# Performance work log

Measured on AMD Instinct MI355X. Metric: run time of the kernel, lower is better.

Reference implementation:

```python
import jax, jax.numpy as jnp
import numpy as np

B, S, D, C = 16, 1024, 768, 2


def setup_inputs() -> dict:
    key = jax.random.key(0)
    ks = jax.random.split(key, 6)
    sc = 1.0 / np.sqrt(D)
    return {
        "tokens": jax.random.normal(ks[0], (B, S, D), jnp.float32),
        "Wk": jax.random.normal(ks[1], (D, D), jnp.float32) * sc,
        "bk": jnp.zeros((D,), jnp.float32),
        "Wq": jax.random.normal(ks[2], (D, D), jnp.float32) * sc,
        "bq": jnp.zeros((D,), jnp.float32),
        "Wv": jax.random.normal(ks[3], (D, D), jnp.float32) * sc,
        "bv": jnp.zeros((D,), jnp.float32),
        "ln_g": jnp.ones((S, D), jnp.float32),
        "ln_b": jnp.zeros((S, D), jnp.float32),
        "W_sgsa": jax.random.normal(ks[4], (D, 1), jnp.float32) * sc,
        "b_sgsa": jnp.zeros((1,), jnp.float32),
        "W_fnn": jax.random.normal(ks[5], (4 * D, C), jnp.float32) * (1.0 / np.sqrt(4 * D)),
        "b_fnn": jnp.zeros((C,), jnp.float32),
    }


def reference(tokens, Wk, bk, Wq, bq, Wv, bv, ln_g, ln_b, W_sgsa, b_sgsa, W_fnn, b_fnn):
    fact = 1.0 / jnp.sqrt(jnp.asarray(D, tokens.dtype))
    # --- token-wise single-head attention ---
    K = tokens @ Wk + bk                                  # [B,S,D]
    Q = tokens @ Wq + bq
    V = tokens @ Wv + bv
    att = jax.nn.softmax(jnp.einsum('bsd,btd->bst', Q, K) * fact, axis=-1)  # [B,S,S]
    out = jnp.einsum('bst,btd->bsd', att, V)              # [B,S,D]
    # --- LayerNorm over last two dims (S,D) jointly, eps=1e-8 ---
    mu = jnp.mean(out, axis=(1, 2), keepdims=True)
    var = jnp.var(out, axis=(1, 2), keepdims=True)
    out_ln = (out - mu) / jnp.sqrt(var + 1e-8) * ln_g + ln_b
    # --- feature-wise attention (same K/Q/V weights, transposed bmm) ---
    K_N = out_ln @ Wk + bk
    Q_N = out_ln @ Wq + bq
    V_N = out_ln @ Wv + bv
    att_N = jax.nn.softmax(jnp.einsum('bsd,bse->bde', Q_N, K_N) * fact, axis=-1)  # [B,D,D]
    out_N = jnp.einsum('bsd,bde->bse', V_N, att_N)        # [B,S,D]
    # --- SGSA gating ---
    gate = out_N @ W_sgsa + b_sgsa                        # [B,S,1]
    out_sgsa = gate * out_N                               # [B,S,D]
    # --- concat, dual pooling, FC ---
    cat = jnp.concatenate([tokens, out_sgsa], axis=2)     # [B,S,2D]
    pooled = jnp.concatenate([jnp.mean(cat, axis=1), jnp.max(cat, axis=1)], axis=1)  # [B,4D]
    return pooled @ W_fnn + b_fnn                         # [B,C]
```

## Files before the change

### kernel.cpp

```cpp
#include <hip/hip_runtime.h>

#define BB 16
#define SS 1024
#define DD 768

typedef _Float16 f16x4 __attribute__((ext_vector_type(4)));
typedef _Float16 f16x8 __attribute__((ext_vector_type(8)));
typedef float f32x4 __attribute__((ext_vector_type(4)));

__device__ __forceinline__ void gload_lds16(const void* g, void* l) {
  __builtin_amdgcn_global_load_lds(
      (const __attribute__((address_space(1))) unsigned int*)g,
      (__attribute__((address_space(3))) unsigned int*)l, 16, 0, 0);
}

template<int OUTM, int BIAS>
__global__ __launch_bounds__(512) void gemm256(
    const _Float16* __restrict__ A, long long aB,
    const _Float16* __restrict__ Bt, long long bB,
    const float* __restrict__ bias, int biasB,
    void* __restrict__ Cv, long long cB,
    float* __restrict__ aux,
    int M, int N, int K)
{
  __shared__ __attribute__((aligned(16))) _Float16 lds[65536];
  const int t = threadIdx.x;
  int z, m0, n0;
  if (OUTM == 3 || OUTM == 4) {
    const int lin = blockIdx.x + 9 * blockIdx.y;
    const int xcd = lin & 7, idx = lin >> 3;
    const int mt  = xcd * 8 + idx / 9;
    const int zn  = idx % 9;
    z  = zn / 3;
    n0 = (zn % 3) * 256;
    m0 = mt * 256;
  } else {
    z = blockIdx.z;
    m0 = blockIdx.x * 256;
    n0 = blockIdx.y * 256;
  }
  const _Float16* Ab = A + (size_t)z * aB;
  const _Float16* Bb = Bt + (size_t)z * bB;

  const int l = t & 63, w = t >> 6;
  const int wr = (w >> 2) * 128, wc = (w & 3) * 64;
  const int lrow = l & 15, kq = l >> 4;
  const int p2v = lrow >> 1;
  const int qread = ((lrow & 1) << 2) | (kq ^ (p2v & 3));
  const int fragoff = p2v * 128 + qread * 16;

  const int sp = t >> 3, sq = t & 7;
  const int srow = 2 * sp + (sq >> 2);
  const int schk = (sq & 3) ^ (sp & 3);
  const size_t ldK = (size_t)K * 2;
  const char* pA0 = (const char*)Ab + (size_t)(m0 + srow) * ldK + schk * 16;
  const char* pA1 = pA0 + (size_t)128 * ldK;
  const char* pB0 = (const char*)Bb + (size_t)(n0 + srow) * ldK + schk * 16;
  const char* pB1 = pB0 + (size_t)128 * ldK;
  char* const ldsb = (char*)lds;
  const int dstt = t * 16;

  auto stg = [&](int mat, int s, int T, int sd) {
    const char* g0 = (mat ? pB0 : pA0) + (size_t)T * 128 + s * 64;
    const char* g1 = (mat ? pB1 : pA1) + (size_t)T * 128 + s * 64;
    char* d = ldsb + sd * 65536 + mat * 32768 + s * 16384 + dstt;
    gload_lds16(g0, d);
    gload_lds16(g1, d + 8192);
  };

  f32x4 acc[8][4] = {};
  f16x8 b0[4], b1[4], a00[4], a01[4], a10[4], a11[4];

  stg(0, 0, 0, 0); stg(1, 0, 0, 0); stg(0, 1, 0, 0); stg(1, 1, 0, 0);

  const int NT = K >> 6;
  for (int T = 0; T < NT; ++T) {
    const int sd = T & 1, sn = sd ^ 1;
    const char* Abase = ldsb + sd * 65536;
    const char* Bbase = Abase + 32768;
    const bool pf = (T + 1) < NT;

    asm volatile("s_waitcnt vmcnt(0)" ::: "memory");
    __builtin_amdgcn_s_barrier();
    asm volatile("" ::: "memory");
    if (pf) {
      stg(0, 0, T + 1, sn); stg(1, 0, T + 1, sn);
      stg(0, 1, T + 1, sn); stg(1, 1, T + 1, sn);
    }

    #pragma unroll
    for (int n = 0; n < 4; n++)
      b0[n]  = *(const f16x8*)(Bbase + (wc + n * 16) * 64 + fragoff);
    #pragma unroll
    for (int mi = 0; mi < 4; mi++)
      a00[mi] = *(const f16x8*)(Abase + (wr + mi * 16) * 64 + fragoff);
    #pragma unroll
    for (int mi = 0; mi < 4; mi++)
      a01[mi] = *(const f16x8*)(Abase + (wr + 64 + mi * 16) * 64 + fragoff);
    #pragma unroll
    for (int n = 0; n < 4; n++)
      b1[n]  = *(const f16x8*)(Bbase + 16384 + (wc + n * 16) * 64 + fragoff);
    #pragma unroll
    for (int mi = 0; mi < 4; mi++)
      a10[mi] = *(const f16x8*)(Abase + 16384 + (wr + mi * 16) * 64 + fragoff);
    #pragma unroll
    for (int mi = 0; mi < 4; mi++)
      a11[mi] = *(const f16x8*)(Abase + 16384 + (wr + 64 + mi * 16) * 64 + fragoff);

    __builtin_amdgcn_s_setprio(1);
    #pragma unroll
    for (int mi = 0; mi < 4; mi++)
      #pragma unroll
      for (int n = 0; n < 4; n++)
        acc[mi][n] = __builtin_amdgcn_mfma_f32_16x16x32_f16(a00[mi], b0[n], acc[mi][n], 0, 0, 0);
    #pragma unroll
    for (int mi = 0; mi < 4; mi++)
      #pragma unroll
      for (int n = 0; n < 4; n++)
        acc[4 + mi][n] = __builtin_amdgcn_mfma_f32_16x16x32_f16(a01[mi], b0[n], acc[4 + mi][n], 0, 0, 0);
    #pragma unroll
    for (int mi = 0; mi < 4; mi++)
      #pragma unroll
      for (int n = 0; n < 4; n++)
        acc[mi][n] = __builtin_amdgcn_mfma_f32_16x16x32_f16(a10[mi], b1[n], acc[mi][n], 0, 0, 0);
    #pragma unroll
    for (int mi = 0; mi < 4; mi++)
      #pragma unroll
      for (int n = 0; n < 4; n++)
        acc[4 + mi][n] = __builtin_amdgcn_mfma_f32_16x16x32_f16(a11[mi], b1[n], acc[4 + mi][n], 0, 0, 0);
    __builtin_amdgcn_s_setprio(0);
  }

  const int crow = (l >> 4) * 4, ccol = l & 15;
  #pragma unroll
  for (int m = 0; m < 8; ++m) {
    const int rq = m0 + wr + (m >> 2) * 64 + (m & 3) * 16 + crow;
    #pragma unroll
    for (int n = 0; n < 4; ++n) {
      const int c = n0 + wc + n * 16 + ccol;
      const float bv = BIAS ? bias[(size_t)z * biasB + c] : 0.0f;
      if (OUTM == 0) {
        float* C = (float*)Cv + (size_t)z * cB;
        #pragma unroll
        for (int j = 0; j < 4; j++)
          C[(size_t)(rq + j) * N + c] = acc[m][n][j] + bv;
      } else if (OUTM == 5 || OUTM == 6) {
        _Float16* C = (_Float16*)Cv + (size_t)z * cB;
        #pragma unroll
        for (int j = 0; j < 4; j++)
          C[(size_t)(rq + j) * N + c] = (_Float16)(acc[m][n][j] + bv);
      } else {
        _Float16* C = (_Float16*)Cv + (size_t)z * cB;
        const bool tr = (OUTM == 3) ? (z == 2) : (z < 2);
        if (tr) {
          const int bq = rq >> 10, s = rq & 1023;
          f16x4 o;
          #pragma unroll
          for (int j = 0; j < 4; j++) o[j] = (_Float16)(acc[m][n][j] + bv);
          *(f16x4*)&C[((size_t)(bq * N + c) << 10) + s] = o;
        } else {
          #pragma unroll
          for (int j = 0; j < 4; j++)
            C[(size_t)(rq + j) * N + c] = (_Float16)(acc[m][n][j] + bv);
        }
      }
    }
  }

  if (OUTM == 6) {
    float ls = 0.0f, lq = 0.0f;
    #pragma unroll
    for (int m = 0; m < 8; ++m)
      #pragma unroll
      for (int n = 0; n < 4; ++n)
        #pragma unroll
        for (int j = 0; j < 4; j++) {
          const float v = acc[m][n][j];
          ls += v; lq += v * v;
        }
    __syncthreads();
    float* red = (float*)lds;
    red[t] = ls; red[512 + t] = lq;
    __syncthreads();
    #pragma unroll
    for (int off = 256; off > 0; off >>= 1) {
      if (t < off) { red[t] += red[t + off]; red[512 + t] += red[512 + t + off]; }
      __syncthreads();
    }
    if (t == 0) {
      const int chunk = blockIdx.x * 3 + blockIdx.y;
      aux[(z * 12 + chunk) * 2]     = red[0];
      aux[(z * 12 + chunk) * 2 + 1] = red[512];
    }
  }
}

__global__ __launch_bounds__(256) void cast_pool(const float* __restrict__ tokens,
                                                 _Float16* __restrict__ tok_h,
                                                 float* __restrict__ tpart)
{
  const int b = blockIdx.y, ch = blockIdx.x, t = threadIdx.x;
  float s0 = 0, s1 = 0, s2 = 0;
  float x0 = -3.4e38f, x1 = -3.4e38f, x2 = -3.4e38f;
  const size_t rowbase = ((size_t)b * SS + ch * 32) * DD;
  for (int i = 0; i < 32; i++) {
    const float* tr = tokens + rowbase + (size_t)i * DD;
    _Float16* hw = tok_h + rowbase + (size_t)i * DD;
    float t0 = tr[t], t1 = tr[t + 256], t2 = tr[t + 512];
    hw[t] = (_Float16)t0; hw[t + 256] = (_Float16)t1; hw[t + 512] = (_Float16)t2;
    s0 += t0; s1 += t1; s2 += t2;
    x0 = fmaxf(x0, t0); x1 = fmaxf(x1, t1); x2 = fmaxf(x2, t2);
  }
  float* pb = tpart + (size_t)(b * 32 + ch) * 1536;
  pb[t] = s0;        pb[t + 256] = s1;        pb[t + 512] = s2;
  pb[768 + t] = x0;  pb[768 + t + 256] = x1;  pb[768 + t + 512] = x2;
}

__global__ __launch_bounds__(256) void transpose_f2h(const float* __restrict__ in,
                                                     _Float16* __restrict__ outp, int R, int C)
{
  __shared__ float tile[32][33];
  const int r0 = blockIdx.y * 32, c0 = blockIdx.x * 32;
  const int tx = threadIdx.x & 31, ty = threadIdx.x >> 5;
  #pragma unroll
  for (int i = 0; i < 4; i++)
    tile[ty + i * 8][tx] = in[(size_t)(r0 + ty + i * 8) * C + c0 + tx];
  __syncthreads();
  #pragma unroll
  for (int i = 0; i < 4; i++)
    outp[(size_t)(c0 + ty + i * 8) * R + r0 + tx] = (_Float16)tile[tx][ty + i * 8];
}

__global__ __launch_bounds__(256) void transpose_b2h(const _Float16* __restrict__ in, long long inB,
                                                     _Float16* __restrict__ outp, long long outB,
                                                     int R, int C)
{
  __shared__ _Float16 tile[32][33];
  const _Float16* ib = in + (size_t)blockIdx.z * inB;
  _Float16* ob = outp + (size_t)blockIdx.z * outB;
  const int r0 = blockIdx.y * 32, c0 = blockIdx.x * 32;
  const int tx = threadIdx.x & 31, ty = threadIdx.x >> 5;
  #pragma unroll
  for (int i = 0; i < 4; i++)
    tile[ty + i * 8][tx] = ib[(size_t)(r0 + ty + i * 8) * C + c0 + tx];
  __syncthreads();
  #pragma unroll
  for (int i = 0; i < 4; i++)
    ob[(size_t)(c0 + ty + i * 8) * R + r0 + tx] = tile[tx][ty + i * 8];
}

__global__ void pack_bias(const float* __restrict__ a, const float* __restrict__ b,
                          const float* __restrict__ c, float* __restrict__ o)
{
  int t = blockIdx.x * 256 + threadIdx.x;
  if (t < 768) o[t] = a[t];
  else if (t < 1536) o[t] = b[t - 768];
  else if (t < 2304) o[t] = c[t - 1536];
}

template<int VPT>
__global__ __launch_bounds__(256) void softmax_f2h(const float* __restrict__ X,
                                                   _Float16* __restrict__ Y,
                                                   int L, float scale)
{
  const size_t base = (size_t)blockIdx.x * L;
  const int t = threadIdx.x;
  float v[VPT];
  float m = -3.4e38f;
  #pragma unroll
  for (int j = 0; j < VPT; j++) { v[j] = X[base + t + j * 256]; m = fmaxf(m, v[j]); }
  __shared__ float red[256];
  red[t] = m; __syncthreads();
  #pragma unroll
  for (int off = 128; off > 0; off >>= 1) {
    if (t < off) red[t] = fmaxf(red[t], red[t + off]);
    __syncthreads();
  }
  m = red[0]; __syncthreads();
  float s = 0.0f;
  #pragma unroll
  for (int j = 0; j < VPT; j++) { v[j] = __expf((v[j] - m) * scale); s += v[j]; }
  red[t] = s; __syncthreads();
  #pragma unroll
  for (int off = 128; off > 0; off >>= 1) {
    if (t < off) red[t] += red[t + off];
    __syncthreads();
  }
  const float inv = 1.0f / red[0];
  #pragma unroll
  for (int j = 0; j < VPT; j++) Y[base + t + j * 256] = (_Float16)(v[j] * inv);
}

__global__ void ln_final(const float* __restrict__ part, float* __restrict__ stats)
{
  const int b = blockIdx.x, t = threadIdx.x;
  float s = 0.0f, q = 0.0f;
  if (t < 12) { s = part[(b * 12 + t) * 2]; q = part[(b * 12 + t) * 2 + 1]; }
  #pragma unroll
  for (int off = 32; off > 0; off >>= 1) { s += __shfl_down(s, off); q += __shfl_down(q, off); }
  if (t == 0) {
    const float invN = 1.0f / (float)(SS * DD);
    float mu = s * invN;
    float var = q * invN - mu * mu;
    stats[b * 2] = mu;
    stats[b * 2 + 1] = rsqrtf(var + 1e-8f);
  }
}

__global__ __launch_bounds__(256) void ln_apply_h(_Float16* __restrict__ data,
                                                  const float* __restrict__ g,
                                                  const float* __restrict__ bta,
                                                  const float* __restrict__ stats)
{
  const long long n4 = (long long)BB * SS * DD / 4;
  const int SD4 = SS * DD / 4;
  for (long long i = (long long)blockIdx.x * 256 + threadIdx.x; i < n4;
       i += (long long)gridDim.x * 256) {
    const int b = (int)(i / SD4);
    const int sd4 = (int)(i - (long long)b * SD4);
    const float mu = stats[b * 2], rs = stats[b * 2 + 1];
    f16x4 v = ((const f16x4*)data)[i];
    float4 gg = ((const float4*)g)[sd4];
    float4 bb = ((const float4*)bta)[sd4];
    f16x4 r;
    r[0] = (_Float16)(((float)v[0] - mu) * rs * gg.x + bb.x);
    r[1] = (_Float16)(((float)v[1] - mu) * rs * gg.y + bb.y);
    r[2] = (_Float16)(((float)v[2] - mu) * rs * gg.z + bb.z);
    r[3] = (_Float16)(((float)v[3] - mu) * rs * gg.w + bb.w);
    ((f16x4*)data)[i] = r;
  }
}

__global__ __launch_bounds__(256) void gate_k(const _Float16* __restrict__ outN,
                                              const float* __restrict__ wsg,
                                              const float* __restrict__ bsg,
                                              float* __restrict__ gate)
{
  const int row = blockIdx.x * 4 + (threadIdx.x >> 6);
  const int l = threadIdx.x & 63;
  const _Float16* src = outN + (size_t)row * DD;
  float s = 0.0f;
  #pragma unroll
  for (int i = 0; i < 12; i++) s += (float)src[l + i * 64] * wsg[l + i * 64];
  #pragma unroll
  for (int off = 32; off > 0; off >>= 1) s += __shfl_down(s, off);
  if (l == 0) gate[row] = s + bsg[0];
}

__global__ __launch_bounds__(256) void opool(const _Float16* __restrict__ outN,
                                             const float* __restrict__ gate,
                                             float* __restrict__ opart)
{
  const int b = blockIdx.y, ch = blockIdx.x, t = threadIdx.x;
  float s0 = 0, s1 = 0, s2 = 0;
  float x0 = -3.4e38f, x1 = -3.4e38f, x2 = -3.4e38f;
  const size_t rowbase = ((size_t)b * SS + ch * 32) * DD;
  for (int i = 0; i < 32; i++) {
    const _Float16* orw = outN + rowbase + (size_t)i * DD;
    const float g = gate[b * SS + ch * 32 + i];
    float o0 = (float)orw[t] * g, o1 = (float)orw[t + 256] * g, o2 = (float)orw[t + 512] * g;
    s0 += o0; s1 += o1; s2 += o2;
    x0 = fmaxf(x0, o0); x1 = fmaxf(x1, o1); x2 = fmaxf(x2, o2);
  }
  float* pb = opart + (size_t)(b * 32 + ch) * 1536;
  pb[t] = s0;        pb[t + 256] = s1;        pb[t + 512] = s2;
  pb[768 + t] = x0;  pb[768 + t + 256] = x1;  pb[768 + t + 512] = x2;
}

__global__ __launch_bounds__(256) void pool_final(const float* __restrict__ tpart,
                                                  const float* __restrict__ opart,
                                                  float* __restrict__ pooled)
{
  const int idx = blockIdx.x * 256 + threadIdx.x;
  const int b = idx / DD, d = idx - b * DD;
  float st = 0, so = 0, xt = -3.4e38f, xo = -3.4e38f;
  for (int ch = 0; ch < 32; ch++) {
    const float* tb = tpart + (size_t)(b * 32 + ch) * 1536;
    const float* ob = opart + (size_t)(b * 32 + ch) * 1536;
    st += tb[d]; xt = fmaxf(xt, tb[768 + d]);
    so += ob[d]; xo = fmaxf(xo, ob[768 + d]);
  }
  const float inv = 1.0f / (float)SS;
  pooled[(size_t)b * 3072 + d]        = st * inv;
  pooled[(size_t)b * 3072 + 768 + d]  = so * inv;
  pooled[(size_t)b * 3072 + 1536 + d] = xt;
  pooled[(size_t)b * 3072 + 2304 + d] = xo;
}

__global__ __launch_bounds__(256) void fc_k(const float* __restrict__ pooled,
                                            const float* __restrict__ Wf,
                                            const float* __restrict__ bf,
                                            float* __restrict__ outp)
{
  const int b = blockIdx.x, t = threadIdx.x;
  float p0 = 0.0f, p1 = 0.0f;
  #pragma unroll
  for (int i = 0; i < 12; i++) {
    const int j = t + i * 256;
    const float pv = pooled[(size_t)b * 3072 + j];
    p0 += pv * Wf[j * 2];
    p1 += pv * Wf[j * 2 + 1];
  }
  __shared__ float r0[256], r1[256];
  r0[t] = p0; r1[t] = p1; __syncthreads();
  #pragma unroll
  for (int off = 128; off > 0; off >>= 1) {
    if (t < off) { r0[t] += r0[t + off]; r1[t] += r1[t + off]; }
    __syncthreads();
  }
  if (t == 0) {
    outp[b * 2 + 0] = r0[0] + bf[0];
    outp[b * 2 + 1] = r1[0] + bf[1];
  }
}

extern "C" void kernel_launch(void* const* d_in, const int* in_sizes, int n_in,
                              void* d_out, int out_size, void* d_ws, size_t ws_size,
                              hipStream_t stream)
{
  const float* tokens = (const float*)d_in[0];
  const float* Wk  = (const float*)d_in[1];
  const float* bk  = (const float*)d_in[2];
  const float* Wq  = (const float*)d_in[3];
  const float* bq  = (const float*)d_in[4];
  const float* Wv  = (const float*)d_in[5];
  const float* bv  = (const float*)d_in[6];
  const float* lng = (const float*)d_in[7];
  const float* lnb = (const float*)d_in[8];
  const float* Wsg = (const float*)d_in[9];
  const float* bsg = (const float*)d_in[10];
  const float* Wf  = (const float*)d_in[11];
  const float* bfn = (const float*)d_in[12];
  float* outp = (float*)d_out;
  (void)in_sizes; (void)n_in; (void)out_size; (void)ws_size;

  char* ws = (char*)d_ws;
  float*    R0   = (float*)(ws + 0);
  _Float16* R1   = (_Float16*)(ws + 67108864);
  _Float16* R2   = (_Float16*)(ws + 92274688);
  _Float16* R3   = (_Float16*)(ws + 117440512);
  _Float16* R4   = (_Float16*)(ws + 142606336);
  _Float16* R5   = (_Float16*)(ws + 167772160);
  _Float16* Wt   = (_Float16*)(ws + 201326592);
  float* bias3   = (float*)(ws + 204865536);
  float* lnpart  = (float*)(ws + 204874752);
  float* stats   = (float*)(ws + 204878848);
  float* gate    = (float*)(ws + 204878976);
  float* tpart   = (float*)(ws + 204944512);
  float* opart   = (float*)(ws + 208090240);
  float* pooled  = (float*)(ws + 211235968);

  const float fact = 0.036084391824351615f;
  const long long SD = (long long)SS * DD;
  const long long S2 = (long long)SS * SS;
  const long long D2 = (long long)DD * DD;
  const long long PL = (long long)BB * SD;

  cast_pool<<<dim3(32, BB), 256, 0, stream>>>(tokens, R1, tpart);
  transpose_f2h<<<dim3(24, 24), 256, 0, stream>>>(Wk, Wt,               768, 768);
  transpose_f2h<<<dim3(24, 24), 256, 0, stream>>>(Wq, Wt + 589824,      768, 768);
  transpose_f2h<<<dim3(24, 24), 256, 0, stream>>>(Wv, Wt + 2 * 589824,  768, 768);
  pack_bias<<<9, 256, 0, stream>>>(bk, bq, bv, bias3);

  gemm256<3, 1><<<dim3(9, 64, 1), 512, 0, stream>>>(R1, 0, Wt, 589824, bias3, 768,
                                                    (void*)R2, PL, nullptr, BB * SS, DD, DD);
  gemm256<0, 0><<<dim3(4, 4, 16), 512, 0, stream>>>(R3, SD, R2, SD, nullptr, 0,
                                                    (void*)R0, S2, nullptr, SS, SS, DD);
  softmax_f2h<4><<<BB * SS, 256, 0, stream>>>(R0, R5, SS, fact);
  gemm256<6, 0><<<dim3(4, 3, 16), 512, 0, stream>>>(R5, S2, R4, SD, nullptr, 0,
                                                    (void*)R1, SD, lnpart, SS, DD, SS);
  ln_final<<<16, 64, 0, stream>>>(lnpart, stats);
  ln_apply_h<<<2048, 256, 0, stream>>>(R1, lng, lnb, stats);

  gemm256<4, 1><<<dim3(9, 64, 1), 512, 0, stream>>>(R1, 0, Wt, 589824, bias3, 768,
                                                    (void*)R2, PL, nullptr, BB * SS, DD, DD);
  gemm256<0, 0><<<dim3(3, 3, 16), 512, 0, stream>>>(R3, SD, R2, SD, nullptr, 0,
                                                    (void*)R0, D2, nullptr, DD, DD, SS);
  softmax_f2h<3><<<BB * DD, 256, 0, stream>>>(R0, R5, DD, fact);
  transpose_b2h<<<dim3(24, 24, 16), 256, 0, stream>>>(R5, D2, R1, D2, DD, DD);
  gemm256<5, 0><<<dim3(4, 3, 16), 512, 0, stream>>>(R4, SD, R1, D2, nullptr, 0,
                                                    (void*)R5, SD, nullptr, SS, DD, DD);

  gate_k<<<4096, 256, 0, stream>>>(R5, Wsg, bsg, gate);
  opool<<<dim3(32, BB), 256, 0, stream>>>(R5, gate, opart);
  pool_final<<<48, 256, 0, stream>>>(tpart, opart, pooled);
  fc_k<<<16, 256, 0, stream>>>(pooled, Wf, bfn, outp);
}
```

Measured before the change: 418.0 us.

## Shrink GEMM tile to 256x128 with K-step 32 and smaller LDS

Restructures the shared GEMM kernel from 256x256 tiles with a K-step of 64 to 256x128 tiles with a K-step of 32. LDS drops from 128KB to 48KB, the accumulators halve, and the kernel sets a minimum of 4 blocks per CU so more blocks can be resident. Grids double in the N dimension and the LayerNorm partial reduction grows to 24 chunks. The aim is better occupancy and less tail imbalance on the small batched GEMMs. The cost is lower arithmetic intensity per tile, more global traffic, twice as many barriers per K, and possible register pressure from the occupancy hint.

```diff
diff --git a/kernel.cpp b/kernel.cpp
--- a/kernel.cpp
+++ b/kernel.cpp
@@ -15,7 +15,7 @@
 }
 
 template<int OUTM, int BIAS>
-__global__ __launch_bounds__(512) void gemm256(
+__global__ __launch_bounds__(512, 4) void gemm256(
     const _Float16* __restrict__ A, long long aB,
     const _Float16* __restrict__ Bt, long long bB,
     const float* __restrict__ bias, int biasB,
@@ -23,118 +23,85 @@
     float* __restrict__ aux,
     int M, int N, int K)
 {
-  __shared__ __attribute__((aligned(16))) _Float16 lds[65536];
+  __shared__ __attribute__((aligned(16))) _Float16 lds[24576];
   const int t = threadIdx.x;
   int z, m0, n0;
   if (OUTM == 3 || OUTM == 4) {
-    const int lin = blockIdx.x + 9 * blockIdx.y;
+    const int lin = blockIdx.x + 18 * blockIdx.y;
     const int xcd = lin & 7, idx = lin >> 3;
-    const int mt  = xcd * 8 + idx / 9;
-    const int zn  = idx % 9;
-    z  = zn / 3;
-    n0 = (zn % 3) * 256;
+    const int mt  = xcd * 8 + idx / 18;
+    const int zn  = idx % 18;
+    z  = zn / 6;
+    n0 = (zn % 6) * 128;
     m0 = mt * 256;
   } else {
     z = blockIdx.z;
     m0 = blockIdx.x * 256;
-    n0 = blockIdx.y * 256;
+    n0 = blockIdx.y * 128;
   }
   const _Float16* Ab = A + (size_t)z * aB;
   const _Float16* Bb = Bt + (size_t)z * bB;
 
   const int l = t & 63, w = t >> 6;
-  const int wr = (w >> 2) * 128, wc = (w & 3) * 64;
+  const int wr = (w >> 1) * 64, wc = (w & 1) * 64;
   const int lrow = l & 15, kq = l >> 4;
-  const int p2v = lrow >> 1;
-  const int qread = ((lrow & 1) << 2) | (kq ^ (p2v & 3));
-  const int fragoff = p2v * 128 + qread * 16;
-
-  const int sp = t >> 3, sq = t & 7;
-  const int srow = 2 * sp + (sq >> 2);
-  const int schk = (sq & 3) ^ (sp & 3);
+  const int fragoff = lrow * 64 + ((kq ^ (lrow & 3)) << 4);
+
+  const int srow = t >> 2;
+  const int schk = (t & 3) ^ ((t >> 2) & 3);
   const size_t ldK = (size_t)K * 2;
   const char* pA0 = (const char*)Ab + (size_t)(m0 + srow) * ldK + schk * 16;
   const char* pA1 = pA0 + (size_t)128 * ldK;
   const char* pB0 = (const char*)Bb + (size_t)(n0 + srow) * ldK + schk * 16;
-  const char* pB1 = pB0 + (size_t)128 * ldK;
   char* const ldsb = (char*)lds;
   const int dstt = t * 16;
 
-  auto stg = [&](int mat, int s, int T, int sd) {
-    const char* g0 = (mat ? pB0 : pA0) + (size_t)T * 128 + s * 64;
-    const char* g1 = (mat ? pB1 : pA1) + (size_t)T * 128 + s * 64;
-    char* d = ldsb + sd * 65536 + mat * 32768 + s * 16384 + dstt;
-    gload_lds16(g0, d);
-    gload_lds16(g1, d + 8192);
+  auto stg = [&](int T, int sd) {
+    const char* ga0 = pA0 + (size_t)T * 64;
+    const char* ga1 = pA1 + (size_t)T * 64;
+    const char* gb  = pB0 + (size_t)T * 64;
+    char* d = ldsb + sd * 24576 + dstt;
+    gload_lds16(ga0, d);
+    gload_lds16(ga1, d + 8192);
+    gload_lds16(gb,  d + 16384);
   };
 
-  f32x4 acc[8][4] = {};
-  f16x8 b0[4], b1[4], a00[4], a01[4], a10[4], a11[4];
-
-  stg(0, 0, 0, 0); stg(1, 0, 0, 0); stg(0, 1, 0, 0); stg(1, 1, 0, 0);
-
-  const int NT = K >> 6;
+  f32x4 acc[4][4] = {};
+  f16x8 af[4], bf[4];
+
+  stg(0, 0);
+
+  const int NT = K >> 5;
   for (int T = 0; T < NT; ++T) {
     const int sd = T & 1, sn = sd ^ 1;
-    const char* Abase = ldsb + sd * 65536;
-    const char* Bbase = Abase + 32768;
-    const bool pf = (T + 1) < NT;
+    const char* Abase = ldsb + sd * 24576;
+    const char* Bbase = Abase + 16384;
 
     asm volatile("s_waitcnt vmcnt(0)" ::: "memory");
     __builtin_amdgcn_s_barrier();
     asm volatile("" ::: "memory");
-    if (pf) {
-      stg(0, 0, T + 1, sn); stg(1, 0, T + 1, sn);
-      stg(0, 1, T + 1, sn); stg(1, 1, T + 1, sn);
-    }
+    if (T + 1 < NT) stg(T + 1, sn);
 
     #pragma unroll
     for (int n = 0; n < 4; n++)
-      b0[n]  = *(const f16x8*)(Bbase + (wc + n * 16) * 64 + fragoff);
+      bf[n] = *(const f16x8*)(Bbase + (wc + n * 16) * 64 + fragoff);
     #pragma unroll
     for (int mi = 0; mi < 4; mi++)
-      a00[mi] = *(const f16x8*)(Abase + (wr + mi * 16) * 64 + fragoff);
-    #pragma unroll
-    for (int mi = 0; mi < 4; mi++)
-      a01[mi] = *(const f16x8*)(Abase + (wr + 64 + mi * 16) * 64 + fragoff);
-    #pragma unroll
-    for (int n = 0; n < 4; n++)
-      b1[n]  = *(const f16x8*)(Bbase + 16384 + (wc + n * 16) * 64 + fragoff);
-    #pragma unroll
-    for (int mi = 0; mi < 4; mi++)
-      a10[mi] = *(const f16x8*)(Abase + 16384 + (wr + mi * 16) * 64 + fragoff);
-    #pragma unroll
-    for (int mi = 0; mi < 4; mi++)
-      a11[mi] = *(const f16x8*)(Abase + 16384 + (wr + 64 + mi * 16) * 64 + fragoff);
+      af[mi] = *(const f16x8*)(Abase + (wr + mi * 16) * 64 + fragoff);
 
     __builtin_amdgcn_s_setprio(1);
     #pragma unroll
     for (int mi = 0; mi < 4; mi++)
       #pragma unroll
       for (int n = 0; n < 4; n++)
-        acc[mi][n] = __builtin_amdgcn_mfma_f32_16x16x32_f16(a00[mi], b0[n], acc[mi][n], 0, 0, 0);
-    #pragma unroll
-    for (int mi = 0; mi < 4; mi++)
-      #pragma unroll
-      for (int n = 0; n < 4; n++)
-        acc[4 + mi][n] = __builtin_amdgcn_mfma_f32_16x16x32_f16(a01[mi], b0[n], acc[4 + mi][n], 0, 0, 0);
-    #pragma unroll
-    for (int mi = 0; mi < 4; mi++)
-      #pragma unroll
-      for (int n = 0; n < 4; n++)
-        acc[mi][n] = __builtin_amdgcn_mfma_f32_16x16x32_f16(a10[mi], b1[n], acc[mi][n], 0, 0, 0);
-    #pragma unroll
-    for (int mi = 0; mi < 4; mi++)
-      #pragma unroll
-      for (int n = 0; n < 4; n++)
-        acc[4 + mi][n] = __builtin_amdgcn_mfma_f32_16x16x32_f16(a11[mi], b1[n], acc[4 + mi][n], 0, 0, 0);
+        acc[mi][n] = __builtin_amdgcn_mfma_f32_16x16x32_f16(af[mi], bf[n], acc[mi][n], 0, 0, 0);
     __builtin_amdgcn_s_setprio(0);
   }
 
   const int crow = (l >> 4) * 4, ccol = l & 15;
   #pragma unroll
-  for (int m = 0; m < 8; ++m) {
-    const int rq = m0 + wr + (m >> 2) * 64 + (m & 3) * 16 + crow;
+  for (int m = 0; m < 4; ++m) {
+    const int rq = m0 + wr + m * 16 + crow;
     #pragma unroll
     for (int n = 0; n < 4; ++n) {
       const int c = n0 + wc + n * 16 + ccol;
@@ -170,7 +137,7 @@
   if (OUTM == 6) {
     float ls = 0.0f, lq = 0.0f;
     #pragma unroll
-    for (int m = 0; m < 8; ++m)
+    for (int m = 0; m < 4; ++m)
       #pragma unroll
       for (int n = 0; n < 4; ++n)
         #pragma unroll
@@ -188,9 +155,9 @@
       __syncthreads();
     }
     if (t == 0) {
-      const int chunk = blockIdx.x * 3 + blockIdx.y;
-      aux[(z * 12 + chunk) * 2]     = red[0];
-      aux[(z * 12 + chunk) * 2 + 1] = red[512];
+      const int chunk = blockIdx.x * 6 + blockIdx.y;
+      aux[(z * 24 + chunk) * 2]     = red[0];
+      aux[(z * 24 + chunk) * 2 + 1] = red[512];
     }
   }
 }
@@ -295,7 +262,7 @@
 {
   const int b = blockIdx.x, t = threadIdx.x;
   float s = 0.0f, q = 0.0f;
-  if (t < 12) { s = part[(b * 12 + t) * 2]; q = part[(b * 12 + t) * 2 + 1]; }
+  if (t < 24) { s = part[(b * 24 + t) * 2]; q = part[(b * 24 + t) * 2 + 1]; }
   #pragma unroll
   for (int off = 32; off > 0; off >>= 1) { s += __shfl_down(s, off); q += __shfl_down(q, off); }
   if (t == 0) {
@@ -462,23 +429,23 @@
   transpose_f2h<<<dim3(24, 24), 256, 0, stream>>>(Wv, Wt + 2 * 589824,  768, 768);
   pack_bias<<<9, 256, 0, stream>>>(bk, bq, bv, bias3);
 
-  gemm256<3, 1><<<dim3(9, 64, 1), 512, 0, stream>>>(R1, 0, Wt, 589824, bias3, 768,
-                                                    (void*)R2, PL, nullptr, BB * SS, DD, DD);
-  gemm256<0, 0><<<dim3(4, 4, 16), 512, 0, stream>>>(R3, SD, R2, SD, nullptr, 0,
+  gemm256<3, 1><<<dim3(18, 64), 512, 0, stream>>>(R1, 0, Wt, 589824, bias3, 768,
+                                                  (void*)R2, PL, nullptr, BB * SS, DD, DD);
+  gemm256<0, 0><<<dim3(4, 8, 16), 512, 0, stream>>>(R3, SD, R2, SD, nullptr, 0,
                                                     (void*)R0, S2, nullptr, SS, SS, DD);
   softmax_f2h<4><<<BB * SS, 256, 0, stream>>>(R0, R5, SS, fact);
-  gemm256<6, 0><<<dim3(4, 3, 16), 512, 0, stream>>>(R5, S2, R4, SD, nullptr, 0,
+  gemm256<6, 0><<<dim3(4, 6, 16), 512, 0, stream>>>(R5, S2, R4, SD, nullptr, 0,
                                                     (void*)R1, SD, lnpart, SS, DD, SS);
   ln_final<<<16, 64, 0, stream>>>(lnpart, stats);
   ln_apply_h<<<2048, 256, 0, stream>>>(R1, lng, lnb, stats);
 
-  gemm256<4, 1><<<dim3(9, 64, 1), 512, 0, stream>>>(R1, 0, Wt, 589824, bias3, 768,
-                                                    (void*)R2, PL, nullptr, BB * SS, DD, DD);
-  gemm256<0, 0><<<dim3(3, 3, 16), 512, 0, stream>>>(R3, SD, R2, SD, nullptr, 0,
+  gemm256<4, 1><<<dim3(18, 64), 512, 0, stream>>>(R1, 0, Wt, 589824, bias3, 768,
+                                                  (void*)R2, PL, nullptr, BB * SS, DD, DD);
+  gemm256<0, 0><<<dim3(3, 6, 16), 512, 0, stream>>>(R3, SD, R2, SD, nullptr, 0,
                                                     (void*)R0, D2, nullptr, DD, DD, SS);
   softmax_f2h<3><<<BB * DD, 256, 0, stream>>>(R0, R5, DD, fact);
   transpose_b2h<<<dim3(24, 24, 16), 256, 0, stream>>>(R5, D2, R1, D2, DD, DD);
-  gemm256<5, 0><<<dim3(4, 3, 16), 512, 0, stream>>>(R4, SD, R1, D2, nullptr, 0,
+  gemm256<5, 0><<<dim3(4, 6, 16), 512, 0, stream>>>(R4, SD, R1, D2, nullptr, 0,
                                                     (void*)R5, SD, nullptr, SS, DD, DD);
 
   gate_k<<<4096, 256, 0, stream>>>(R5, Wsg, bsg, gate);
```

Result: no change. 420.7 us (+0.6%).
